# Kernel optimization log

Hardware: AMD Instinct MI355X
Metric: run time of the kernel (lower is better)

The kernel has to match this reference:

```python
import jax, jax.numpy as jnp
import numpy as np

K = 128      # knowledge_n
E = 4096     # exer_n
S = 2048     # student_n
M = 512      # number of supervised exercises (ex_id)
NUM_UPDATE = 3
THRESHOLD = 0.05
H = 1.0


def setup_inputs() -> dict:
    key = jax.random.key(0)
    ks = jax.random.split(key, 16)
    U_embeding = jax.random.uniform(ks[0], (S, K), dtype=jnp.float32)
    W = jax.random.uniform(ks[1], (K, E), dtype=jnp.float32)
    beiTa_1 = jax.random.uniform(ks[2], (K, E), dtype=jnp.float32)
    beiTa_2 = jax.random.uniform(ks[3], (E, 1), dtype=jnp.float32)
    B = jax.random.uniform(ks[4], (K, E, K), dtype=jnp.float32)
    guess_slip = jax.random.normal(ks[5], (E, 2), dtype=jnp.float32)
    A_emb = jax.random.normal(ks[6], (E, 3), dtype=jnp.float32)
    gamma_c = jax.random.normal(ks[7], (E, 1), dtype=jnp.float32)
    gamma_e = jax.random.normal(ks[8], (E, 1), dtype=jnp.float32)
    alpha = jax.random.normal(ks[9], (E, 1), dtype=jnp.float32)
    score = jax.random.randint(ks[10], (E, 1), 0, 2).astype(jnp.float32)
    user_k_kc = (jax.random.uniform(ks[11], (K, E)) < 0.3).astype(jnp.float32)
    # multi-hot question->concept map, ~4 concepts per exercise, at least 1
    q_kn = (jax.random.uniform(ks[12], (E, K)) < 4.0 / K).astype(jnp.float32)
    q_kn = q_kn.at[jnp.arange(E), jax.random.randint(ks[13], (E,), 0, K)].set(1.0)
    d = q_kn.sum(axis=1, keepdims=True)  # exercise degree, >= 1
    ex_id = jax.random.randint(ks[14], (M,), 0, E, dtype=jnp.int32)
    kn_id = jnp.arange(K, dtype=jnp.int32)
    stu_id = 7
    return dict(U_embeding=U_embeding, W=W, beiTa_1=beiTa_1, beiTa_2=beiTa_2,
                B=B, guess_slip=guess_slip, A_emb=A_emb, gamma_c=gamma_c,
                gamma_e=gamma_e, alpha=alpha, score=score, user_k_kc=user_k_kc,
                q_kn=q_kn, d=d, stu_id=stu_id, kn_id=kn_id, ex_id=ex_id)


def reference(U_embeding, W, beiTa_1, beiTa_2, B, guess_slip, A_emb,
              gamma_c, gamma_e, alpha, score, user_k_kc, q_kn, d,
              stu_id, kn_id, ex_id):
    # The torch loop `for cur_kn in kn_id: update(cur_kn, U_update[num-1])` is a
    # Jacobi sweep: every concept update reads the PREVIOUS state, so all
    # concepts can be computed in one vectorized pass per iteration.
    Bdiag = jnp.einsum('kek->ke', B)           # B[k, e, k], (K, E)
    dvec = d[:, 0]                              # (E,)
    sc = score[:, 0]                            # (E,)
    upd = jnp.zeros((K,), dtype=bool).at[kn_id].set(True)

    def step(u):                                # u: (K,) current mastery state
        # ---- Ic (eq. 7): per-exercise interaction term ----
        su = q_kn @ u                           # (E,)  sum of mastered concepts
        yc = jnp.exp(-(sc - su / dvec) ** 2)    # (E,)
        Pc = jnp.concatenate([1.0 - guess_slip, yc[:, None]], axis=1)  # (E,3)
        Ic = jax.nn.sigmoid(-jnp.sum(A_emb * Pc, axis=1))              # (E,)
        # ---- Gkc: masked, dead-zoned neighbour influence ----
        # U_gkc entries with q_kn==0 are set to 0.5, and column cur_kn is
        # zeroed; dead-zone of 0.5 contributes 0, so it reduces to a gated
        # product with the k-diagonal term subtracted out.
        dv = jnp.where(jnp.abs(u - 0.5) > THRESHOLD, u - 0.5, 0.0)      # (K,)
        qdv = q_kn * dv                         # (E, K)
        Gsum = jnp.einsum('kej,ej->ke', B, qdv) - Bdiag * qdv.T         # (K, E)
        # NOTE: the original subtracts 0.5 twice (sigmoid(...) - 0.5 then
        # reshape(...) - 0.5); replicated faithfully.
        Gkc = jax.nn.sigmoid(-Gsum) - 1.0       # (K, E)
        # ---- Zc ----
        Zc = jax.nn.sigmoid(-(gamma_c[:, 0] / dvec) * (sc - 0.5)) - 0.5  # (E,)
        # ---- WKC and the per-concept contraction over the exercise set ----
        WK = H * Ic[None, :] * (beiTa_1 * Gkc + (beiTa_2[:, 0] * Zc)[None, :])
        s = jnp.sum(user_k_kc * W * WK, axis=1)  # ragged set via 0/1 mask, (K,)
        u_new = jax.nn.sigmoid(-s)
        return jnp.where(upd, u_new, u)

    u0 = U_embeding[stu_id]                     # (K,)
    states = [u0]
    diffs = []
    for _ in range(NUM_UPDATE):
        un = step(states[-1])
        diffs.append(jnp.linalg.norm(un - states[-1]))
        states.append(un)

    state_last = states[-1][:, None]            # U_update[-2] in torch indexing
    state_2nd_last = states[-2][:, None]        # U_update[-3]
    diff_norm = jnp.stack(diffs)

    # ---- supervised predict ----
    Ukse = (q_kn[ex_id] @ state_last) / d[ex_id] - 0.5                  # (M,1)
    predict = jax.nn.sigmoid(-(alpha[ex_id] * Ukse + gamma_e[ex_id]))   # (M,1)
    return (state_last, state_2nd_last, predict, diff_norm)
```

## Files before the change

### kernel.cpp

```cpp
#include <hip/hip_runtime.h>
#include <math.h>

#define KK 128
#define EE 4096
#define MM 512
#define CP 32

#define OFF_U    0
#define OFF_PA   128
#define OFF_PB   2176
#define OFF_CNT  4224
#define OFF_IDX  8320
#define OFF_IDXT 41088
#define OFF_PE   73856
#define OFF_GW   94336
#define OFF_HW   618624
#define OFF_BC   1142912

__global__ __launch_bounds__(256) void k_setup(
    const float* __restrict__ U, const float* __restrict__ W,
    const float* __restrict__ beiTa_1, const float* __restrict__ beiTa_2,
    const float* __restrict__ guess_slip, const float* __restrict__ A_emb,
    const float* __restrict__ gamma_c, const float* __restrict__ score,
    const float* __restrict__ ukc, const float* __restrict__ q_kn,
    const float* __restrict__ d, const int* __restrict__ stu_id,
    float* __restrict__ ws)
{
    int tid = threadIdx.x;
    int blk = blockIdx.x;
    if (blk < 16) {
        int e = blk * 256 + tid;
        int* cnt = (int*)(ws + OFF_CNT);
        signed char* idx  = (signed char*)(ws + OFF_IDX);
        signed char* idxT = (signed char*)(ws + OFF_IDXT);
        float* P01  = ws + OFF_PE;
        float* a2   = P01 + EE;
        float* scv  = a2 + EE;
        float* invd = scv + EE;
        float* bz   = invd + EE;

        int* ip32 = (int*)(idx + e * CP);
        #pragma unroll
        for (int t = 0; t < CP / 4; t++) ip32[t] = -1;
        const float4* qrow = (const float4*)(q_kn + (size_t)e * KK);
        int c = 0;
        for (int j4 = 0; j4 < KK / 4; j4++) {
            float4 q = qrow[j4];
            int j = j4 * 4;
            if (q.x > 0.5f) { if (c < CP) idx[e*CP+c] = (signed char)j;     c++; }
            if (q.y > 0.5f) { if (c < CP) idx[e*CP+c] = (signed char)(j+1); c++; }
            if (q.z > 0.5f) { if (c < CP) idx[e*CP+c] = (signed char)(j+2); c++; }
            if (q.w > 0.5f) { if (c < CP) idx[e*CP+c] = (signed char)(j+3); c++; }
        }
        c = (c < CP) ? c : CP;
        cnt[e] = c;
        for (int i = 0; i < CP; i++) idxT[(size_t)i * EE + e] = idx[e * CP + i];

        float id_ = 1.0f / d[e];
        invd[e] = id_;
        float scr = score[e];
        scv[e] = scr;
        P01[e] = A_emb[3*e] * (1.0f - guess_slip[2*e]) +
                 A_emb[3*e+1] * (1.0f - guess_slip[2*e+1]);
        a2[e] = A_emb[3*e+2];
        float zc = 1.0f / (1.0f + __expf(gamma_c[e] * id_ * (scr - 0.5f))) - 0.5f;
        bz[e] = beiTa_2[e] * zc;

        if (blk == 0 && tid < KK) ws[tid] = U[(size_t)stu_id[0] * KK + tid];
    } else {
        float* gW = ws + OFF_GW;
        float* hW = ws + OFF_HW;
        int stride = 128 * 256;
        for (int t = (blk - 16) * 256 + tid; t < KK * EE; t += stride) {
            float uw = ukc[t] * W[t];
            hW[t] = uw;
            gW[t] = uw * beiTa_1[t];
        }
    }
}

__global__ __launch_bounds__(256) void k_compact(const float* __restrict__ B,
                                                 float* __restrict__ ws)
{
    __shared__ float lds[64 * KK];
    int tid = threadIdx.x;
    int k  = blockIdx.y;
    int e0 = blockIdx.x * 64;

    const float4* src = (const float4*)(B + ((size_t)k * EE + e0) * KK);
    float4* dst4 = (float4*)lds;
    #pragma unroll
    for (int it = 0; it < 8; it++)
        dst4[it * 256 + tid] = src[it * 256 + tid];
    __syncthreads();

    const signed char* idxT = (const signed char*)(ws + OFF_IDXT);
    int eo = tid & 63;
    float* BcB = ws + OFF_BC + (size_t)k * CP * EE + e0 + eo;
    for (int i = tid >> 6; i < CP; i += 4) {
        int j = idxT[(size_t)i * EE + e0 + eo];
        unsigned long long m = __ballot(j >= 0);
        if (!m) break;
        if (j >= 0) BcB[(size_t)i * EE] = lds[eo * KK + j];
    }
}

__global__ __launch_bounds__(256) void k_phase(
    float* __restrict__ ws, float* __restrict__ out,
    const float* __restrict__ pin, float* __restrict__ pout, int phase)
{
    __shared__ float lu[KK];
    __shared__ float sdv[KK];
    __shared__ float red2[KK];
    __shared__ float wred[4];
    int tid = threadIdx.x;
    int ec = blockIdx.x;
    int k  = blockIdx.y;
    int e  = ec * 256 + tid;

    if (tid < KK) {
        float uv;
        if (phase == 0) {
            uv = ws[tid];
        } else {
            float s = 0.0f;
            const float* p = pin + tid * 16;
            #pragma unroll
            for (int t = 0; t < 16; t++) s += p[t];
            uv = 1.0f / (1.0f + __expf(s));
        }
        lu[tid] = uv;
        float t = uv - 0.5f;
        sdv[tid] = (fabsf(t) > 0.05f) ? t : 0.0f;
    }
    __syncthreads();

    const int* cnt = (const int*)(ws + OFF_CNT);
    const signed char* idxT = (const signed char*)(ws + OFF_IDXT);
    const float* P01  = ws + OFF_PE;
    const float* a2   = P01 + EE;
    const float* scv  = a2 + EE;
    const float* invd = scv + EE;
    const float* bzv  = invd + EE;
    const float* gW   = ws + OFF_GW;
    const float* hW   = ws + OFF_HW;
    const float* Bc   = ws + OFF_BC;

    int c = cnt[e];
    const signed char* it = idxT + e;
    const float* bp = Bc + (size_t)k * CP * EE + e;
    float su = 0.0f, gs = 0.0f;
    for (int i = 0; i < c; i++) {
        int j   = it[(size_t)i * EE];
        float b = bp[(size_t)i * EE];
        su += lu[j];
        gs = fmaf(b, (j != k) ? sdv[j] : 0.0f, gs);
    }
    float t0 = scv[e] - su * invd[e];
    float yc = __expf(-t0 * t0);
    float Ic = 1.0f / (1.0f + __expf(P01[e] + a2[e] * yc));
    float Gkc = 1.0f / (1.0f + __expf(gs)) - 1.0f;
    size_t o = (size_t)k * EE + e;
    float v = Ic * (gW[o] * Gkc + hW[o] * bzv[e]);

    #pragma unroll
    for (int m = 1; m < 64; m <<= 1) v += __shfl_xor(v, m);
    if ((tid & 63) == 0) wred[tid >> 6] = v;
    __syncthreads();
    if (tid == 0) pout[k * 16 + ec] = wred[0] + wred[1] + wred[2] + wred[3];

    if (phase >= 1 && blockIdx.x == 0 && blockIdx.y == 0) {
        if (tid < KK) {
            float dd = lu[tid] - ws[tid];
            red2[tid] = dd * dd;
        }
        __syncthreads();
        for (int s2 = 64; s2 > 0; s2 >>= 1) {
            if (tid < s2) red2[tid] += red2[tid + s2];
            __syncthreads();
        }
        if (tid == 0) out[768 + (phase - 1)] = sqrtf(red2[0]);
        if (tid < KK) {
            ws[tid] = lu[tid];
            if (phase == 2) out[128 + tid] = lu[tid];
        }
    }
}

__global__ __launch_bounds__(512) void k_final(
    float* __restrict__ ws, float* __restrict__ out, const float* __restrict__ pin,
    const int* __restrict__ ex_id, const float* __restrict__ alpha,
    const float* __restrict__ gamma_e)
{
    __shared__ float un_s[KK];
    __shared__ float red[KK];
    int tid = threadIdx.x;
    if (tid < KK) {
        float s = 0.0f;
        const float* p = pin + tid * 16;
        #pragma unroll
        for (int t = 0; t < 16; t++) s += p[t];
        float un = 1.0f / (1.0f + __expf(s));
        float dd = un - ws[tid];
        red[tid] = dd * dd;
        un_s[tid] = un;
        out[tid] = un;
    }
    __syncthreads();
    for (int s2 = 64; s2 > 0; s2 >>= 1) {
        if (tid < s2) red[tid] += red[tid + s2];
        __syncthreads();
    }
    if (tid == 0) out[770] = sqrtf(red[0]);

    const int* cnt = (const int*)(ws + OFF_CNT);
    const signed char* idx = (const signed char*)(ws + OFF_IDX);
    const float* invd = ws + OFF_PE + 3 * EE;
    int e = ex_id[tid];
    int c = cnt[e];
    const signed char* ip = idx + (size_t)e * CP;
    float su = 0.0f;
    for (int i = 0; i < c; i++) su += un_s[ip[i]];
    float Ukse = su * invd[e] - 0.5f;
    out[256 + tid] = 1.0f / (1.0f + __expf(alpha[e] * Ukse + gamma_e[e]));
}

extern "C" void kernel_launch(void* const* d_in, const int* in_sizes, int n_in,
                              void* d_out, int out_size, void* d_ws, size_t ws_size,
                              hipStream_t stream) {
    const float* U          = (const float*)d_in[0];
    const float* W          = (const float*)d_in[1];
    const float* beiTa_1    = (const float*)d_in[2];
    const float* beiTa_2    = (const float*)d_in[3];
    const float* B          = (const float*)d_in[4];
    const float* guess_slip = (const float*)d_in[5];
    const float* A_emb      = (const float*)d_in[6];
    const float* gamma_c    = (const float*)d_in[7];
    const float* gamma_e    = (const float*)d_in[8];
    const float* alpha      = (const float*)d_in[9];
    const float* score      = (const float*)d_in[10];
    const float* ukc        = (const float*)d_in[11];
    const float* q_kn       = (const float*)d_in[12];
    const float* d          = (const float*)d_in[13];
    const int*   stu_id     = (const int*)d_in[14];
    const int*   ex_id      = (const int*)d_in[16];
    float* out = (float*)d_out;
    float* ws  = (float*)d_ws;
    float* pA = ws + OFF_PA;
    float* pB = ws + OFF_PB;

    k_setup<<<144, 256, 0, stream>>>(U, W, beiTa_1, beiTa_2, guess_slip, A_emb,
                                     gamma_c, score, ukc, q_kn, d, stu_id, ws);
    k_compact<<<dim3(EE / 64, KK), 256, 0, stream>>>(B, ws);
    k_phase<<<dim3(16, 128), 256, 0, stream>>>(ws, out, pA, pA, 0);
    k_phase<<<dim3(16, 128), 256, 0, stream>>>(ws, out, pA, pB, 1);
    k_phase<<<dim3(16, 128), 256, 0, stream>>>(ws, out, pB, pA, 2);
    k_final<<<1, 512, 0, stream>>>(ws, out, pA, ex_id, alpha, gamma_e);
}
```

Measured before the change: 447.4 us.

## Fuse compact, three Jacobi phases and final predict into one persistent kernel with grid barriers

Replaces the five separate launches (compact, three phase sweeps, final) with one persistent kernel of 1024 blocks that loops over the compaction work and then synchronises between phases through a hierarchical atomic grid barrier. Each block now handles two 256-wide exercise chunks per concept, so the partial-sum layout shrinks from 16 to 8 partials per concept. The aim is to remove per-launch overhead and kernel-boundary drains. The cost is spin-wait barrier latency, and correctness depends on all 1024 blocks being co-resident, which the 4-blocks-per-CU launch bound is meant to ensure.

```diff
diff --git a/kernel.cpp b/kernel.cpp
--- a/kernel.cpp
+++ b/kernel.cpp
@@ -5,10 +5,12 @@
 #define EE 4096
 #define MM 512
 #define CP 32
+#define NB 1024
 
 #define OFF_U    0
 #define OFF_PA   128
 #define OFF_PB   2176
+#define OFF_BAR  3200
 #define OFF_CNT  4224
 #define OFF_IDX  8320
 #define OFF_IDXT 41088
@@ -66,7 +68,11 @@
         float zc = 1.0f / (1.0f + __expf(gamma_c[e] * id_ * (scr - 0.5f))) - 0.5f;
         bz[e] = beiTa_2[e] * zc;
 
-        if (blk == 0 && tid < KK) ws[tid] = U[(size_t)stu_id[0] * KK + tid];
+        if (blk == 0) {
+            if (tid < KK) ws[tid] = U[(size_t)stu_id[0] * KK + tid];
+            unsigned* bar = (unsigned*)(ws + OFF_BAR);
+            for (int t = tid; t < 544; t += 256) bar[t] = 0u;
+        }
     } else {
         float* gW = ws + OFF_GW;
         float* hW = ws + OFF_HW;
@@ -79,61 +85,42 @@
     }
 }
 
-__global__ __launch_bounds__(256) void k_compact(const float* __restrict__ B,
-                                                 float* __restrict__ ws)
+__device__ __forceinline__ void gridbar(unsigned* bar, int bid)
+{
+    __syncthreads();
+    if (threadIdx.x == 0) {
+        __threadfence();
+        unsigned* gctr = bar + (bid >> 5) * 16;
+        unsigned* mctr = bar + 512;
+        unsigned* gen  = bar + 528;
+        unsigned g = __hip_atomic_load(gen, __ATOMIC_RELAXED, __HIP_MEMORY_SCOPE_AGENT);
+        bool release = false;
+        if (__hip_atomic_fetch_add(gctr, 1u, __ATOMIC_ACQ_REL, __HIP_MEMORY_SCOPE_AGENT) == 31u) {
+            __hip_atomic_store(gctr, 0u, __ATOMIC_RELAXED, __HIP_MEMORY_SCOPE_AGENT);
+            if (__hip_atomic_fetch_add(mctr, 1u, __ATOMIC_ACQ_REL, __HIP_MEMORY_SCOPE_AGENT) == 31u) {
+                __hip_atomic_store(mctr, 0u, __ATOMIC_RELAXED, __HIP_MEMORY_SCOPE_AGENT);
+                __hip_atomic_store(gen, g + 1u, __ATOMIC_RELEASE, __HIP_MEMORY_SCOPE_AGENT);
+                release = true;
+            }
+        }
+        if (!release) {
+            while (__hip_atomic_load(gen, __ATOMIC_ACQUIRE, __HIP_MEMORY_SCOPE_AGENT) == g)
+                __builtin_amdgcn_s_sleep(1);
+        }
+        __threadfence();
+    }
+    __syncthreads();
+}
+
+__global__ __launch_bounds__(256, 4) void k_mega(
+    const float* __restrict__ B, float* __restrict__ ws, float* __restrict__ out,
+    const int* __restrict__ ex_id, const float* __restrict__ alpha,
+    const float* __restrict__ gamma_e)
 {
     __shared__ float lds[64 * KK];
     int tid = threadIdx.x;
-    int k  = blockIdx.y;
-    int e0 = blockIdx.x * 64;
-
-    const float4* src = (const float4*)(B + ((size_t)k * EE + e0) * KK);
-    float4* dst4 = (float4*)lds;
-    #pragma unroll
-    for (int it = 0; it < 8; it++)
-        dst4[it * 256 + tid] = src[it * 256 + tid];
-    __syncthreads();
-
-    const signed char* idxT = (const signed char*)(ws + OFF_IDXT);
-    int eo = tid & 63;
-    float* BcB = ws + OFF_BC + (size_t)k * CP * EE + e0 + eo;
-    for (int i = tid >> 6; i < CP; i += 4) {
-        int j = idxT[(size_t)i * EE + e0 + eo];
-        unsigned long long m = __ballot(j >= 0);
-        if (!m) break;
-        if (j >= 0) BcB[(size_t)i * EE] = lds[eo * KK + j];
-    }
-}
-
-__global__ __launch_bounds__(256) void k_phase(
-    float* __restrict__ ws, float* __restrict__ out,
-    const float* __restrict__ pin, float* __restrict__ pout, int phase)
-{
-    __shared__ float lu[KK];
-    __shared__ float sdv[KK];
-    __shared__ float red2[KK];
-    __shared__ float wred[4];
-    int tid = threadIdx.x;
-    int ec = blockIdx.x;
-    int k  = blockIdx.y;
-    int e  = ec * 256 + tid;
-
-    if (tid < KK) {
-        float uv;
-        if (phase == 0) {
-            uv = ws[tid];
-        } else {
-            float s = 0.0f;
-            const float* p = pin + tid * 16;
-            #pragma unroll
-            for (int t = 0; t < 16; t++) s += p[t];
-            uv = 1.0f / (1.0f + __expf(s));
-        }
-        lu[tid] = uv;
-        float t = uv - 0.5f;
-        sdv[tid] = (fabsf(t) > 0.05f) ? t : 0.0f;
-    }
-    __syncthreads();
+    int bid = blockIdx.x;
+    unsigned* bar = (unsigned*)(ws + OFF_BAR);
 
     const int* cnt = (const int*)(ws + OFF_CNT);
     const signed char* idxT = (const signed char*)(ws + OFF_IDXT);
@@ -144,85 +131,136 @@
     const float* bzv  = invd + EE;
     const float* gW   = ws + OFF_GW;
     const float* hW   = ws + OFF_HW;
-    const float* Bc   = ws + OFF_BC;
-
-    int c = cnt[e];
-    const signed char* it = idxT + e;
-    const float* bp = Bc + (size_t)k * CP * EE + e;
-    float su = 0.0f, gs = 0.0f;
-    for (int i = 0; i < c; i++) {
-        int j   = it[(size_t)i * EE];
-        float b = bp[(size_t)i * EE];
-        su += lu[j];
-        gs = fmaf(b, (j != k) ? sdv[j] : 0.0f, gs);
-    }
-    float t0 = scv[e] - su * invd[e];
-    float yc = __expf(-t0 * t0);
-    float Ic = 1.0f / (1.0f + __expf(P01[e] + a2[e] * yc));
-    float Gkc = 1.0f / (1.0f + __expf(gs)) - 1.0f;
-    size_t o = (size_t)k * EE + e;
-    float v = Ic * (gW[o] * Gkc + hW[o] * bzv[e]);
-
-    #pragma unroll
-    for (int m = 1; m < 64; m <<= 1) v += __shfl_xor(v, m);
-    if ((tid & 63) == 0) wred[tid >> 6] = v;
+    float* Bc = ws + OFF_BC;
+    float* pA = ws + OFF_PA;
+    float* pB = ws + OFF_PB;
+
+    for (int unit = bid; unit < KK * 64; unit += NB) {
+        int k  = unit >> 6;
+        int e0 = (unit & 63) << 6;
+        const float4* src = (const float4*)(B + ((size_t)k * EE + e0) * KK);
+        float4* dst4 = (float4*)lds;
+        #pragma unroll
+        for (int it = 0; it < 8; it++)
+            dst4[it * 256 + tid] = src[it * 256 + tid];
+        __syncthreads();
+        int eo = tid & 63;
+        float* BcB = Bc + (size_t)k * CP * EE + e0 + eo;
+        for (int i = tid >> 6; i < CP; i += 4) {
+            int j = idxT[(size_t)i * EE + e0 + eo];
+            unsigned long long m = __ballot(j >= 0);
+            if (!m) break;
+            if (j >= 0) BcB[(size_t)i * EE] = lds[eo * KK + j];
+        }
+        __syncthreads();
+    }
+    gridbar(bar, bid);
+
+    float* lu   = lds;
+    float* sdv  = lds + 128;
+    float* red2 = lds + 256;
+    float* wred = lds + 384;
+    int k  = bid & 127;
+    int ec = bid >> 7;
+
+    for (int p = 0; p < 3; p++) {
+        const float* pin = (p == 2) ? pB : pA;
+        float* pout      = (p == 1) ? pB : pA;
+
+        if (tid < KK) {
+            float uv;
+            if (p == 0) {
+                uv = ws[tid];
+            } else {
+                float s = 0.0f;
+                const float* pp = pin + tid * 8;
+                #pragma unroll
+                for (int t = 0; t < 8; t++) s += pp[t];
+                uv = 1.0f / (1.0f + __expf(s));
+            }
+            lu[tid] = uv;
+            float t = uv - 0.5f;
+            sdv[tid] = (fabsf(t) > 0.05f) ? t : 0.0f;
+        }
+        __syncthreads();
+
+        float vacc = 0.0f;
+        #pragma unroll
+        for (int sub = 0; sub < 2; sub++) {
+            int e = ec * 512 + sub * 256 + tid;
+            int c = cnt[e];
+            const signed char* it = idxT + e;
+            const float* bp = Bc + (size_t)k * CP * EE + e;
+            float su = 0.0f, gs = 0.0f;
+            for (int i = 0; i < c; i++) {
+                int j   = it[(size_t)i * EE];
+                float b = bp[(size_t)i * EE];
+                su += lu[j];
+                gs = fmaf(b, (j != k) ? sdv[j] : 0.0f, gs);
+            }
+            float t0 = scv[e] - su * invd[e];
+            float yc = __expf(-t0 * t0);
+            float Ic = 1.0f / (1.0f + __expf(P01[e] + a2[e] * yc));
+            float Gkc = 1.0f / (1.0f + __expf(gs)) - 1.0f;
+            size_t o = (size_t)k * EE + e;
+            vacc += Ic * (gW[o] * Gkc + hW[o] * bzv[e]);
+        }
+        #pragma unroll
+        for (int m = 1; m < 64; m <<= 1) vacc += __shfl_xor(vacc, m);
+        if ((tid & 63) == 0) wred[tid >> 6] = vacc;
+        __syncthreads();
+        if (tid == 0) pout[k * 8 + ec] = wred[0] + wred[1] + wred[2] + wred[3];
+
+        if (bid == 0 && p >= 1) {
+            if (tid < KK) {
+                float dd = lu[tid] - ws[tid];
+                red2[tid] = dd * dd;
+            }
+            __syncthreads();
+            for (int s2 = 64; s2 > 0; s2 >>= 1) {
+                if (tid < s2) red2[tid] += red2[tid + s2];
+                __syncthreads();
+            }
+            if (tid == 0) out[768 + (p - 1)] = sqrtf(red2[0]);
+            if (tid < KK) {
+                ws[tid] = lu[tid];
+                if (p == 2) out[128 + tid] = lu[tid];
+            }
+        }
+        gridbar(bar, bid);
+    }
+
+    if (bid >= 2) return;
+    if (tid < KK) {
+        float s = 0.0f;
+        const float* pp = pA + tid * 8;
+        #pragma unroll
+        for (int t = 0; t < 8; t++) s += pp[t];
+        float un = 1.0f / (1.0f + __expf(s));
+        lu[tid] = un;
+        if (bid == 0) {
+            float dd = un - ws[tid];
+            red2[tid] = dd * dd;
+            out[tid] = un;
+        }
+    }
     __syncthreads();
-    if (tid == 0) pout[k * 16 + ec] = wred[0] + wred[1] + wred[2] + wred[3];
-
-    if (phase >= 1 && blockIdx.x == 0 && blockIdx.y == 0) {
-        if (tid < KK) {
-            float dd = lu[tid] - ws[tid];
-            red2[tid] = dd * dd;
-        }
-        __syncthreads();
+    if (bid == 0) {
         for (int s2 = 64; s2 > 0; s2 >>= 1) {
             if (tid < s2) red2[tid] += red2[tid + s2];
             __syncthreads();
         }
-        if (tid == 0) out[768 + (phase - 1)] = sqrtf(red2[0]);
-        if (tid < KK) {
-            ws[tid] = lu[tid];
-            if (phase == 2) out[128 + tid] = lu[tid];
-        }
-    }
-}
-
-__global__ __launch_bounds__(512) void k_final(
-    float* __restrict__ ws, float* __restrict__ out, const float* __restrict__ pin,
-    const int* __restrict__ ex_id, const float* __restrict__ alpha,
-    const float* __restrict__ gamma_e)
-{
-    __shared__ float un_s[KK];
-    __shared__ float red[KK];
-    int tid = threadIdx.x;
-    if (tid < KK) {
-        float s = 0.0f;
-        const float* p = pin + tid * 16;
-        #pragma unroll
-        for (int t = 0; t < 16; t++) s += p[t];
-        float un = 1.0f / (1.0f + __expf(s));
-        float dd = un - ws[tid];
-        red[tid] = dd * dd;
-        un_s[tid] = un;
-        out[tid] = un;
-    }
-    __syncthreads();
-    for (int s2 = 64; s2 > 0; s2 >>= 1) {
-        if (tid < s2) red[tid] += red[tid + s2];
-        __syncthreads();
-    }
-    if (tid == 0) out[770] = sqrtf(red[0]);
-
-    const int* cnt = (const int*)(ws + OFF_CNT);
+        if (tid == 0) out[770] = sqrtf(red2[0]);
+    }
     const signed char* idx = (const signed char*)(ws + OFF_IDX);
-    const float* invd = ws + OFF_PE + 3 * EE;
-    int e = ex_id[tid];
+    int m = bid * 256 + tid;
+    int e = ex_id[m];
     int c = cnt[e];
     const signed char* ip = idx + (size_t)e * CP;
     float su = 0.0f;
-    for (int i = 0; i < c; i++) su += un_s[ip[i]];
+    for (int i = 0; i < c; i++) su += lu[ip[i]];
     float Ukse = su * invd[e] - 0.5f;
-    out[256 + tid] = 1.0f / (1.0f + __expf(alpha[e] * Ukse + gamma_e[e]));
+    out[256 + m] = 1.0f / (1.0f + __expf(alpha[e] * Ukse + gamma_e[e]));
 }
 
 extern "C" void kernel_launch(void* const* d_in, const int* in_sizes, int n_in,
@@ -246,14 +284,8 @@
     const int*   ex_id      = (const int*)d_in[16];
     float* out = (float*)d_out;
     float* ws  = (float*)d_ws;
-    float* pA = ws + OFF_PA;
-    float* pB = ws + OFF_PB;
 
     k_setup<<<144, 256, 0, stream>>>(U, W, beiTa_1, beiTa_2, guess_slip, A_emb,
                                      gamma_c, score, ukc, q_kn, d, stu_id, ws);
-    k_compact<<<dim3(EE / 64, KK), 256, 0, stream>>>(B, ws);
-    k_phase<<<dim3(16, 128), 256, 0, stream>>>(ws, out, pA, pA, 0);
-    k_phase<<<dim3(16, 128), 256, 0, stream>>>(ws, out, pA, pB, 1);
-    k_phase<<<dim3(16, 128), 256, 0, stream>>>(ws, out, pB, pA, 2);
-    k_final<<<1, 512, 0, stream>>>(ws, out, pA, ex_id, alpha, gamma_e);
-}
+    k_mega<<<NB, 256, 0, stream>>>(B, ws, out, ex_id, alpha, gamma_e);
+}
```

New measurement: 960.5 us. +114.7%, slower.

## Fuse B compaction with first Jacobi phase and widen setup grid

Applied to the files above, without the earlier changes.

Merges the B-diagonal gather kernel with phase 0 of the Jacobi sweep, so each block compacts its own 256 exercises for one concept and then runs the first update step on them. This removes one launch and lets phase 0 read compacted B that was just written, while it is likely still in cache. The setup kernel's grid is also doubled to spread the elementwise W/beiTa_1 preprocessing over more blocks. In exchange, each fused block now loops over four 64-exercise tiles in sequence with extra barriers, which gives fewer, longer blocks for the bandwidth-heavy B read.

```diff
diff --git a/kernel.cpp b/kernel.cpp
--- a/kernel.cpp
+++ b/kernel.cpp
@@ -16,6 +16,7 @@
 #define OFF_GW   94336
 #define OFF_HW   618624
 #define OFF_BC   1142912
+
 
 __global__ __launch_bounds__(256) void k_setup(
     const float* __restrict__ U, const float* __restrict__ W,
@@ -70,7 +71,7 @@
     } else {
         float* gW = ws + OFF_GW;
         float* hW = ws + OFF_HW;
-        int stride = 128 * 256;
+        int stride = 256 * 256;
         for (int t = (blk - 16) * 256 + tid; t < KK * EE; t += stride) {
             float uw = ukc[t] * W[t];
             hW[t] = uw;
@@ -79,30 +80,79 @@
     }
 }
 
-__global__ __launch_bounds__(256) void k_compact(const float* __restrict__ B,
-                                                 float* __restrict__ ws)
+__global__ __launch_bounds__(256) void k_cp0(
+    const float* __restrict__ B, float* __restrict__ ws, float* __restrict__ pout)
 {
     __shared__ float lds[64 * KK];
     int tid = threadIdx.x;
+    int ec = blockIdx.x;
     int k  = blockIdx.y;
-    int e0 = blockIdx.x * 64;
-
-    const float4* src = (const float4*)(B + ((size_t)k * EE + e0) * KK);
-    float4* dst4 = (float4*)lds;
+
+    const signed char* idxT = (const signed char*)(ws + OFF_IDXT);
+    float* Bc = ws + OFF_BC;
+
+    for (int t4 = 0; t4 < 4; t4++) {
+        int e0 = ec * 256 + t4 * 64;
+        const float4* src = (const float4*)(B + ((size_t)k * EE + e0) * KK);
+        float4* dst4 = (float4*)lds;
+        #pragma unroll
+        for (int it = 0; it < 8; it++)
+            dst4[it * 256 + tid] = src[it * 256 + tid];
+        __syncthreads();
+        int eo = tid & 63;
+        float* BcB = Bc + (size_t)k * CP * EE + e0 + eo;
+        for (int i = tid >> 6; i < CP; i += 4) {
+            int j = idxT[(size_t)i * EE + e0 + eo];
+            unsigned long long m = __ballot(j >= 0);
+            if (!m) break;
+            if (j >= 0) BcB[(size_t)i * EE] = lds[eo * KK + j];
+        }
+        __syncthreads();
+    }
+
+    float* lu   = lds;
+    float* sdv  = lds + 128;
+    float* wred = lds + 256;
+    if (tid < KK) {
+        float uv = ws[tid];
+        lu[tid] = uv;
+        float t = uv - 0.5f;
+        sdv[tid] = (fabsf(t) > 0.05f) ? t : 0.0f;
+    }
+    __syncthreads();
+
+    const int* cnt = (const int*)(ws + OFF_CNT);
+    const float* P01  = ws + OFF_PE;
+    const float* a2   = P01 + EE;
+    const float* scv  = a2 + EE;
+    const float* invd = scv + EE;
+    const float* bzv  = invd + EE;
+    const float* gW   = ws + OFF_GW;
+    const float* hW   = ws + OFF_HW;
+
+    int e = ec * 256 + tid;
+    int c = cnt[e];
+    const signed char* it = idxT + e;
+    const float* bp = Bc + (size_t)k * CP * EE + e;
+    float su = 0.0f, gs = 0.0f;
+    for (int i = 0; i < c; i++) {
+        int j   = it[(size_t)i * EE];
+        float b = bp[(size_t)i * EE];
+        su += lu[j];
+        gs = fmaf(b, (j != k) ? sdv[j] : 0.0f, gs);
+    }
+    float t0 = scv[e] - su * invd[e];
+    float yc = __expf(-t0 * t0);
+    float Ic = 1.0f / (1.0f + __expf(P01[e] + a2[e] * yc));
+    float Gkc = 1.0f / (1.0f + __expf(gs)) - 1.0f;
+    size_t o = (size_t)k * EE + e;
+    float v = Ic * (gW[o] * Gkc + hW[o] * bzv[e]);
+
     #pragma unroll
-    for (int it = 0; it < 8; it++)
-        dst4[it * 256 + tid] = src[it * 256 + tid];
-    __syncthreads();
-
-    const signed char* idxT = (const signed char*)(ws + OFF_IDXT);
-    int eo = tid & 63;
-    float* BcB = ws + OFF_BC + (size_t)k * CP * EE + e0 + eo;
-    for (int i = tid >> 6; i < CP; i += 4) {
-        int j = idxT[(size_t)i * EE + e0 + eo];
-        unsigned long long m = __ballot(j >= 0);
-        if (!m) break;
-        if (j >= 0) BcB[(size_t)i * EE] = lds[eo * KK + j];
-    }
+    for (int m = 1; m < 64; m <<= 1) v += __shfl_xor(v, m);
+    if ((tid & 63) == 0) wred[tid >> 6] = v;
+    __syncthreads();
+    if (tid == 0) pout[k * 16 + ec] = wred[0] + wred[1] + wred[2] + wred[3];
 }
 
 __global__ __launch_bounds__(256) void k_phase(
@@ -119,16 +169,11 @@
     int e  = ec * 256 + tid;
 
     if (tid < KK) {
-        float uv;
-        if (phase == 0) {
-            uv = ws[tid];
-        } else {
-            float s = 0.0f;
-            const float* p = pin + tid * 16;
-            #pragma unroll
-            for (int t = 0; t < 16; t++) s += p[t];
-            uv = 1.0f / (1.0f + __expf(s));
-        }
+        float s = 0.0f;
+        const float* p = pin + tid * 16;
+        #pragma unroll
+        for (int t = 0; t < 16; t++) s += p[t];
+        float uv = 1.0f / (1.0f + __expf(s));
         lu[tid] = uv;
         float t = uv - 0.5f;
         sdv[tid] = (fabsf(t) > 0.05f) ? t : 0.0f;
@@ -169,7 +214,7 @@
     __syncthreads();
     if (tid == 0) pout[k * 16 + ec] = wred[0] + wred[1] + wred[2] + wred[3];
 
-    if (phase >= 1 && blockIdx.x == 0 && blockIdx.y == 0) {
+    if (blockIdx.x == 0 && blockIdx.y == 0) {
         if (tid < KK) {
             float dd = lu[tid] - ws[tid];
             red2[tid] = dd * dd;
@@ -249,10 +294,9 @@
     float* pA = ws + OFF_PA;
     float* pB = ws + OFF_PB;
 
-    k_setup<<<144, 256, 0, stream>>>(U, W, beiTa_1, beiTa_2, guess_slip, A_emb,
+    k_setup<<<272, 256, 0, stream>>>(U, W, beiTa_1, beiTa_2, guess_slip, A_emb,
                                      gamma_c, score, ukc, q_kn, d, stu_id, ws);
-    k_compact<<<dim3(EE / 64, KK), 256, 0, stream>>>(B, ws);
-    k_phase<<<dim3(16, 128), 256, 0, stream>>>(ws, out, pA, pA, 0);
+    k_cp0<<<dim3(16, 128), 256, 0, stream>>>(B, ws, pA);
     k_phase<<<dim3(16, 128), 256, 0, stream>>>(ws, out, pA, pB, 1);
     k_phase<<<dim3(16, 128), 256, 0, stream>>>(ws, out, pB, pA, 2);
     k_final<<<1, 512, 0, stream>>>(ws, out, pA, ex_id, alpha, gamma_e);
```

Measured after the change: 457.0 us. 1.02x slower.
